# Performance work log

Hardware: AMD Instinct MI355X
Metric: run time of the kernel (lower is better)

The kernel has to match this reference:

```python
import jax, jax.numpy as jnp
import numpy as np

B = 512       # number of graphs
MAX_N = 128   # pad length (>= max(num_atoms))
D = 256       # emb_dim


def setup_inputs() -> dict:
    key = jax.random.key(0)
    ks = jax.random.split(key, 20)
    num_atoms_np = np.full(B, 80, dtype=np.int64)
    num_atoms_np[: B // 2] = 112
    num_atoms_np[B // 2 :] = 48
    total = int(num_atoms_np.sum())  # 40960, static
    scale = 1.0 / np.sqrt(D)

    def lin_w(k):
        return jax.random.normal(k, (D, D), jnp.float32) * scale

    inp = {
        'rep_2d': jax.random.normal(ks[0], (total, D), jnp.float32),
        'rep_3d': jax.random.normal(ks[1], (total, D), jnp.float32),
        'num_atoms': jnp.asarray(num_atoms_np),
        # mha_2d_3d (queries from 2d, keys/values from 3d)
        'wq23': lin_w(ks[2]), 'bq23': jnp.zeros((D,), jnp.float32),
        'wk23': lin_w(ks[3]), 'bk23': jnp.zeros((D,), jnp.float32),
        'wv23': lin_w(ks[4]), 'bv23': jnp.zeros((D,), jnp.float32),
        # mha_3d_2d (queries from 3d, keys/values from 2d)
        'wq32': lin_w(ks[5]), 'bq32': jnp.zeros((D,), jnp.float32),
        'wk32': lin_w(ks[6]), 'bk32': jnp.zeros((D,), jnp.float32),
        'wv32': lin_w(ks[7]), 'bv32': jnp.zeros((D,), jnp.float32),
        # per-branch Linear (normalizer=Identity) + GELU
        'wm23': lin_w(ks[8]), 'bm23': jnp.zeros((D,), jnp.float32),
        'wm32': lin_w(ks[9]), 'bm32': jnp.zeros((D,), jnp.float32),
    }
    return inp


def _variadic_to_padded(flat, num_atoms):
    # flat: [total, D] -> padded [B, MAX_N, D], mask [B, MAX_N] (True = valid)
    cum = jnp.cumsum(num_atoms)
    offsets = cum - num_atoms
    pos = jnp.arange(MAX_N)
    mask = pos[None, :] < num_atoms[:, None]
    idx = jnp.where(mask, offsets[:, None] + pos[None, :], 0)
    padded = flat[idx] * mask[..., None].astype(flat.dtype)
    return padded, mask


def _padded_to_variadic(padded, num_atoms, total):
    # padded: [B, MAX_N, D] -> flat [total, D]
    cum = jnp.cumsum(num_atoms)
    t = jnp.arange(total)
    b = jnp.searchsorted(cum, t, side='right')
    i = t - (cum - num_atoms)[b]
    return padded[b, i]


def _cross_attn(q_in, kv_in, mask, wq, bq, wk, bk, wv, bv):
    # single-head scaled dot-product cross-attention, key-side padding mask
    q = q_in @ wq.T + bq
    k = kv_in @ wk.T + bk
    v = kv_in @ wv.T + bv
    s = jnp.einsum('bqd,bkd->bqk', q, k) / jnp.sqrt(jnp.asarray(D, q.dtype))
    s = jnp.where(mask[:, None, :], s, jnp.asarray(-1e9, s.dtype))
    a = jax.nn.softmax(s, axis=-1)
    return jnp.einsum('bqk,bkd->bqd', a, v)


def reference(rep_2d, rep_3d, num_atoms,
              wq23, bq23, wk23, bk23, wv23, bv23,
              wq32, bq32, wk32, bk32, wv32, bv32,
              wm23, bm23, wm32, bm32):
    total = rep_2d.shape[0]
    p2d, mask = _variadic_to_padded(rep_2d, num_atoms)
    p3d, _ = _variadic_to_padded(rep_3d, num_atoms)
    x2d = _cross_attn(p2d, p3d, mask, wq23, bq23, wk23, bk23, wv23, bv23)
    x3d = _cross_attn(p3d, p2d, mask, wq32, bq32, wk32, bk32, wv32, bv32)
    x2d = _padded_to_variadic(x2d, num_atoms, total)
    x3d = _padded_to_variadic(x3d, num_atoms, total)
    out2d = jax.nn.gelu(x2d @ wm23.T + bm23, approximate=False)
    out3d = jax.nn.gelu(x3d @ wm32.T + bm32, approximate=False)
    return (out2d, out3d)
```

## Files before the change

kernel.cpp:

```cpp
#include <hip/hip_runtime.h>
#include <hip/hip_bf16.h>
#include <cstdint>


typedef short s16x8 __attribute__((ext_vector_type(8)));
typedef float f32x4 __attribute__((ext_vector_type(4)));

__device__ __forceinline__ s16x8 cvt8(const float* p) {
  float4 a0 = *(const float4*)p, a1 = *(const float4*)(p + 4);
  union { s16x8 v; __bf16 e[8]; } u;
  u.e[0] = (__bf16)a0.x; u.e[1] = (__bf16)a0.y; u.e[2] = (__bf16)a0.z; u.e[3] = (__bf16)a0.w;
  u.e[4] = (__bf16)a1.x; u.e[5] = (__bf16)a1.y; u.e[6] = (__bf16)a1.z; u.e[7] = (__bf16)a1.w;
  return u.v;
}
__device__ __forceinline__ float fast_gelu(float x) {
  float ax = fabsf(x);
  float t = 1.0f / (1.0f + 0.3275911f * (ax * 0.70710678f));
  float y = t * (0.254829592f + t * (-0.284496736f + t * (1.421413741f +
            t * (-1.453152027f + t * 1.061405429f))));
  float er = 1.0f - y * __expf(-0.5f * ax * ax);
  er = (x < 0.f) ? -er : er;
  return 0.5f * x * (1.0f + er);
}

__global__ void sentinel_kernel(float* out, float v) {
  if (threadIdx.x == 0 && blockIdx.x == 0) out[0] = v;
}

__global__ __launch_bounds__(512) void scan_kernel(
    const int* __restrict__ na, int* __restrict__ offs,
    int B, int total, float* out)
{
  __shared__ int s32[512];
  __shared__ int s64[512];
  const int t = threadIdx.x;
  int v32 = 0, v64 = 0;
  if (t < B) {
    v32 = na[t];
    v64 = (int)((const long long*)na)[t];
  }
  s32[t] = v32; s64[t] = v64;
  __syncthreads();
  for (int o = 1; o < 512; o <<= 1) {
    int a = (t >= o) ? s32[t - o] : 0;
    int b = (t >= o) ? s64[t - o] : 0;
    __syncthreads();
    s32[t] += a; s64[t] += b;
    __syncthreads();
  }
  int tot32 = s32[B - 1], tot64 = s64[B - 1];
  bool ok32 = (tot32 == total), ok64 = (tot64 == total);
  if (t < B) offs[t] = ok32 ? (s32[t] - v32) : ok64 ? (s64[t] - v64) : 0;
  if (t == 0) {
    offs[B] = ok32 ? tot32 : ok64 ? tot64 : 0;
    if (!ok32 && !ok64) out[0] = 31337.0f;
  }
}

__global__ __launch_bounds__(256) void cvt2_kernel(
    const float* __restrict__ in0, const float* __restrict__ in1,
    __bf16* __restrict__ out0, __bf16* __restrict__ out1) {
  const float* in = blockIdx.y ? in1 : in0;
  __bf16* out = blockIdx.y ? out1 : out0;
  int i = (blockIdx.x * 256 + threadIdx.x) * 4;
  float4 f = *(const float4*)(in + i);
  out[i + 0] = (__bf16)f.x; out[i + 1] = (__bf16)f.y;
  out[i + 2] = (__bf16)f.z; out[i + 3] = (__bf16)f.w;
}

__global__ __launch_bounds__(256) void gemm_kernel(
    const float* __restrict__ A, const float* __restrict__ Bw,
    const float* __restrict__ bias, __bf16* __restrict__ C, int N)
{
  __shared__ __bf16 At[128 * 32];
  __shared__ __bf16 Bt[128 * 32];
  const int t = threadIdx.x;
  const int lane = t & 63, w = t >> 6;
  const int wr = w >> 1, wc = w & 1;
  const int l15 = lane & 15, l4 = lane >> 4;
  const int by = blockIdx.x, bx = blockIdx.y;

  f32x4 acc[4][4];
  for (int m = 0; m < 4; ++m)
    for (int nn = 0; nn < 4; ++nn) acc[m][nn] = (f32x4){0.f, 0.f, 0.f, 0.f};

  for (int kk = 0; kk < 256; kk += 32) {
    for (int j = 0; j < 2; ++j) {
      int c = t + j * 256;
      int row = c >> 2, off0 = (c & 3) * 8;
      *(s16x8*)(&At[row * 32 + off0]) = cvt8(A + (size_t)(by * 128 + row) * 256 + kk + off0);
      *(s16x8*)(&Bt[row * 32 + off0]) = cvt8(Bw + (size_t)(bx * 128 + row) * 256 + kk + off0);
    }
    __syncthreads();
    s16x8 af[4], bfr[4];
    for (int m = 0; m < 4; ++m)
      af[m] = *(const s16x8*)(&At[(wr * 64 + m * 16 + l15) * 32 + l4 * 8]);
    for (int nn = 0; nn < 4; ++nn)
      bfr[nn] = *(const s16x8*)(&Bt[(wc * 64 + nn * 16 + l15) * 32 + l4 * 8]);
    for (int m = 0; m < 4; ++m)
      for (int nn = 0; nn < 4; ++nn)
        acc[m][nn] = __builtin_amdgcn_mfma_f32_16x16x32_bf16(af[m], bfr[nn], acc[m][nn], 0, 0, 0);
    __syncthreads();
  }

  for (int m = 0; m < 4; ++m) {
    int row0 = by * 128 + wr * 64 + m * 16 + l4 * 4;
    for (int nn = 0; nn < 4; ++nn) {
      int col = bx * 128 + wc * 64 + nn * 16 + l15;
      float bc = bias[col];
      for (int r = 0; r < 4; ++r) {
        int row = row0 + r;
        C[(size_t)row * N + col] = (__bf16)(acc[m][nn][r] + bc);
      }
    }
  }
}

#define CTP 136
__global__ __launch_bounds__(256) void vgemm_kernel(
    const float* __restrict__ A, const float* __restrict__ Bw,
    const float* __restrict__ bias, __bf16* __restrict__ Vt, int total)
{
  __shared__ __bf16 At[128 * 32];
  __shared__ __bf16 Bt[128 * 32];
  __shared__ __bf16 Ct[128 * CTP];
  const int t = threadIdx.x;
  const int lane = t & 63, w = t >> 6;
  const int wr = w >> 1, wc = w & 1;
  const int l15 = lane & 15, l4 = lane >> 4;
  const int by = blockIdx.x, bx = blockIdx.y;

  f32x4 acc[4][4];
  for (int m = 0; m < 4; ++m)
    for (int nn = 0; nn < 4; ++nn) acc[m][nn] = (f32x4){0.f, 0.f, 0.f, 0.f};

  for (int kk = 0; kk < 256; kk += 32) {
    for (int j = 0; j < 2; ++j) {
      int c = t + j * 256;
      int row = c >> 2, off0 = (c & 3) * 8;
      *(s16x8*)(&At[row * 32 + off0]) = cvt8(A + (size_t)(by * 128 + row) * 256 + kk + off0);
      *(s16x8*)(&Bt[row * 32 + off0]) = cvt8(Bw + (size_t)(bx * 128 + row) * 256 + kk + off0);
    }
    __syncthreads();
    s16x8 af[4], bfr[4];
    for (int m = 0; m < 4; ++m)
      af[m] = *(const s16x8*)(&At[(wr * 64 + m * 16 + l15) * 32 + l4 * 8]);
    for (int nn = 0; nn < 4; ++nn)
      bfr[nn] = *(const s16x8*)(&Bt[(wc * 64 + nn * 16 + l15) * 32 + l4 * 8]);
    for (int m = 0; m < 4; ++m)
      for (int nn = 0; nn < 4; ++nn)
        acc[m][nn] = __builtin_amdgcn_mfma_f32_16x16x32_bf16(af[m], bfr[nn], acc[m][nn], 0, 0, 0);
    __syncthreads();
  }

  for (int m = 0; m < 4; ++m) {
    int rl0 = wr * 64 + m * 16 + l4 * 4;
    for (int nn = 0; nn < 4; ++nn) {
      int cl = wc * 64 + nn * 16 + l15;
      for (int r = 0; r < 4; ++r) {
        int rl = rl0 + r;
        Ct[rl * CTP + cl] = (__bf16)(acc[m][nn][r] + bias[by * 128 + rl]);
      }
    }
  }
  __syncthreads();

  for (int i = 0; i < 8; ++i) {
    int c = t + i * 256;
    int tile = c >> 5, w5 = c & 31;
    int kb_l = tile >> 3, db_l = tile & 7;
    int d_l = w5 & 15, kh = w5 >> 4;
    *(uint4*)(Vt + (((size_t)(bx * 8 + kb_l) * 16 + (by * 8 + db_l)) << 8) + w5 * 8) =
        *(const uint4*)(&Ct[(db_l * 16 + d_l) * CTP + kb_l * 16 + kh * 8]);
  }
}

struct Attn2Args {
  const __bf16* Q[2]; const __bf16* K[2]; const __bf16* V[2];
  unsigned long long X[2];
};
#define KP 264
#define PP 136
#define XP 272
__global__ __launch_bounds__(512, 2) void attn2_kernel(
    Attn2Args args, const int* __restrict__ offs, int total)
{
  __shared__ __bf16 smem[128 * 136];
  __bf16 (*Klds)[KP] = (__bf16(*)[KP])smem;
  __bf16 (*Plds)[PP] = (__bf16(*)[PP])smem;
  __bf16 (*XT)[XP]   = (__bf16(*)[XP])smem;

  const int br = blockIdx.y;
  const __bf16* Q  = args.Q[br];
  const __bf16* Km = args.K[br];
  const __bf16* Vt = args.V[br];
  __bf16* X = (__bf16*)args.X[br];

  const int g = blockIdx.x;
  const int off = offs[g];
  const int n = offs[g + 1] - off;
  const int t = threadIdx.x, lane = t & 63, w = t >> 6;
  const int l15 = lane & 15, l4 = lane >> 4;
  const bool qact = (w * 16) < n;
  const bool big = (n > 64);

  const int srow = t >> 5, scol = (t & 31) * 16;
  uint4 kst[4];
  #pragma unroll
  for (int j = 0; j < 4; ++j)
    kst[j] = *(const uint4*)((const char*)(Km + (size_t)(off + j * 16 + srow) * 256) + scol);
  s16x8 qf[8];
  if (qact) {
    int qr = w * 16 + l15; if (qr >= n) qr = n - 1;
    const __bf16* qp = Q + (size_t)(off + qr) * 256 + l4 * 8;
    #pragma unroll
    for (int kk = 0; kk < 8; ++kk) qf[kk] = *(const s16x8*)(qp + kk * 32);
  }
  #pragma unroll
  for (int j = 0; j < 4; ++j)
    *(uint4*)((char*)&Klds[j * 16 + srow][0] + scol) = kst[j];
  uint4 kst1[4];
  if (big) {
    #pragma unroll
    for (int j = 0; j < 4; ++j)
      kst1[j] = *(const uint4*)((const char*)(Km + (size_t)(off + 64 + j * 16 + srow) * 256) + scol);
  }
  __syncthreads();

  f32x4 sacc[8];
  #pragma unroll
  for (int i = 0; i < 8; ++i) sacc[i] = (f32x4){0.f, 0.f, 0.f, 0.f};
  if (qact) {
    #pragma unroll
    for (int kt = 0; kt < 4; ++kt) {
      const __bf16* kp = &Klds[kt * 16 + l15][l4 * 8];
      #pragma unroll
      for (int kk = 0; kk < 8; ++kk) {
        s16x8 kf = *(const s16x8*)(kp + kk * 32);
        sacc[kt] = __builtin_amdgcn_mfma_f32_16x16x32_bf16(qf[kk], kf, sacc[kt], 0, 0, 0);
      }
    }
  }
  __syncthreads();
  if (big) {
    #pragma unroll
    for (int j = 0; j < 4; ++j)
      *(uint4*)((char*)&Klds[j * 16 + srow][0] + scol) = kst1[j];
    __syncthreads();
    if (qact) {
      #pragma unroll
      for (int kt = 0; kt < 4; ++kt) {
        const __bf16* kp = &Klds[kt * 16 + l15][l4 * 8];
        #pragma unroll
        for (int kk = 0; kk < 8; ++kk) {
          s16x8 kf = *(const s16x8*)(kp + kk * 32);
          sacc[4 + kt] = __builtin_amdgcn_mfma_f32_16x16x32_bf16(qf[kk], kf, sacc[4 + kt], 0, 0, 0);
        }
      }
    }
    __syncthreads();
  }

  if (qact) {
    #pragma unroll
    for (int r = 0; r < 4; ++r) {
      float sv[8];
      float m = -1e30f;
      #pragma unroll
      for (int kt = 0; kt < 8; ++kt) {
        int key = kt * 16 + l15;
        float v = (key < n) ? sacc[kt][r] * 0.0625f : -1e30f;
        sv[kt] = v; m = fmaxf(m, v);
      }
      for (int o = 1; o < 16; o <<= 1) m = fmaxf(m, __shfl_xor(m, o));
      float p[8], sum = 0.f;
      #pragma unroll
      for (int kt = 0; kt < 8; ++kt) { p[kt] = __expf(sv[kt] - m); sum += p[kt]; }
      for (int o = 1; o < 16; o <<= 1) sum += __shfl_xor(sum, o);
      float inv = 1.f / sum;
      int q = w * 16 + l4 * 4 + r;
      #pragma unroll
      for (int kt = 0; kt < 4; ++kt)
        Plds[q][kt * 16 + l15] = (__bf16)(p[kt] * inv);
      if (big) {
        #pragma unroll
        for (int kt = 4; kt < 8; ++kt)
          Plds[q][kt * 16 + l15] = (__bf16)(p[kt] * inv);
      }
    }
  }
  __syncthreads();

  const int dbase = w * 32;
  const int ktiles = total >> 4;
  f32x4 xacc[2][8];
  #pragma unroll
  for (int dt = 0; dt < 2; ++dt)
    #pragma unroll
    for (int qm = 0; qm < 8; ++qm) xacc[dt][qm] = (f32x4){0.f, 0.f, 0.f, 0.f};

  #pragma unroll
  for (int dt = 0; dt < 2; ++dt) {
    int db = w * 2 + dt;
    s16x8 vf[4];
    #pragma unroll
    for (int ks = 0; ks < 4; ++ks) {
      int kb = (off >> 4) + ks * 2 + (l4 >> 1);
      if (kb >= ktiles) kb = ktiles - 1;
      vf[ks] = *(const s16x8*)(Vt + (((size_t)kb * 16 + db) << 8)
                               + (l15 + ((l4 & 1) << 4)) * 8);
    }
    #pragma unroll
    for (int qm = 0; qm < 8; ++qm) {
      #pragma unroll
      for (int ks = 0; ks < 4; ++ks) {
        if (ks * 32 < n) {
          s16x8 pa = *(const s16x8*)(&Plds[qm * 16 + l15][ks * 32 + l4 * 8]);
          xacc[dt][qm] = __builtin_amdgcn_mfma_f32_16x16x32_bf16(pa, vf[ks], xacc[dt][qm], 0, 0, 0);
        }
      }
    }
  }
  __syncthreads();

  #pragma unroll
  for (int dt = 0; dt < 2; ++dt)
    #pragma unroll
    for (int qm = 0; qm < 4; ++qm)
      #pragma unroll
      for (int r = 0; r < 4; ++r)
        XT[qm * 16 + l4 * 4 + r][dbase + dt * 16 + l15] = (__bf16)xacc[dt][qm][r];
  __syncthreads();
  #pragma unroll
  for (int i = 0; i < 4; ++i) {
    int c = t + i * 512;
    int row = c >> 5, seg = c & 31;
    if (row < n)
      *(uint4*)(X + (size_t)(off + row) * 256 + seg * 8) =
          *(const uint4*)(&XT[row][seg * 8]);
  }
  if (big) {
    __syncthreads();
    #pragma unroll
    for (int dt = 0; dt < 2; ++dt)
      #pragma unroll
      for (int qm = 4; qm < 8; ++qm)
        #pragma unroll
        for (int r = 0; r < 4; ++r)
          XT[(qm - 4) * 16 + l4 * 4 + r][dbase + dt * 16 + l15] = (__bf16)xacc[dt][qm][r];
    __syncthreads();
    #pragma unroll
    for (int i = 0; i < 4; ++i) {
      int c = t + i * 512;
      int row = c >> 5, seg = c & 31;
      int grow = 64 + row;
      if (grow < n)
        *(uint4*)(X + (size_t)(off + grow) * 256 + seg * 8) =
            *(const uint4*)(&XT[row][seg * 8]);
    }
  }
}

#define OP 88
__global__ __launch_bounds__(256) void gemm_out(
    const __bf16* __restrict__ A, const __bf16* __restrict__ W,
    const float* __restrict__ bias, float* __restrict__ C)
{
  __shared__ __bf16 At[64 * OP];
  __shared__ __bf16 Bt[128 * OP];
  const int t = threadIdx.x;
  const int lane = t & 63, w = t >> 6;
  const int wr = w >> 1, wc = w & 1;
  const int l15 = lane & 15, l4 = lane >> 4;
  const int by = blockIdx.x, bx = blockIdx.y;

  f32x4 acc[2][4];
  for (int m = 0; m < 2; ++m)
    for (int nn = 0; nn < 4; ++nn) acc[m][nn] = (f32x4){0.f, 0.f, 0.f, 0.f};

  for (int kk = 0; kk < 256; kk += 64) {
    #pragma unroll
    for (int j = 0; j < 2; ++j) {
      int c = t + j * 256;
      int row = c >> 3, off0 = (c & 7) * 8;
      *(s16x8*)(&At[row * OP + off0]) =
          *(const s16x8*)(A + (size_t)(by * 64 + row) * 256 + kk + off0);
    }
    #pragma unroll
    for (int j = 0; j < 4; ++j) {
      int c = t + j * 256;
      int row = c >> 3, off0 = (c & 7) * 8;
      *(s16x8*)(&Bt[row * OP + off0]) =
          *(const s16x8*)(W + (size_t)(bx * 128 + row) * 256 + kk + off0);
    }
    __syncthreads();
    #pragma unroll
    for (int k2 = 0; k2 < 2; ++k2) {
      s16x8 af[2], bfr[4];
      #pragma unroll
      for (int m = 0; m < 2; ++m)
        af[m] = *(const s16x8*)(&At[(wr * 32 + m * 16 + l15) * OP + k2 * 32 + l4 * 8]);
      #pragma unroll
      for (int nn = 0; nn < 4; ++nn)
        bfr[nn] = *(const s16x8*)(&Bt[(wc * 64 + nn * 16 + l15) * OP + k2 * 32 + l4 * 8]);
      #pragma unroll
      for (int m = 0; m < 2; ++m)
        #pragma unroll
        for (int nn = 0; nn < 4; ++nn)
          acc[m][nn] = __builtin_amdgcn_mfma_f32_16x16x32_bf16(af[m], bfr[nn], acc[m][nn], 0, 0, 0);
    }
    __syncthreads();
  }

  for (int m = 0; m < 2; ++m) {
    int row0 = by * 64 + wr * 32 + m * 16 + l4 * 4;
    for (int nn = 0; nn < 4; ++nn) {
      int col = bx * 128 + wc * 64 + nn * 16 + l15;
      float bc = bias[col];
      for (int r = 0; r < 4; ++r) {
        int row = row0 + r;
        C[(size_t)row * 256 + col] = fast_gelu(acc[m][nn][r] + bc);
      }
    }
  }
}

extern "C" void kernel_launch(void* const* d_in, const int* in_sizes, int n_in,
                              void* d_out, int out_size, void* d_ws, size_t ws_size,
                              hipStream_t stream) {
  const float* rep2d = (const float*)d_in[0];
  const float* rep3d = (const float*)d_in[1];
  const int*   na    = (const int*)d_in[2];
  const float* wq23 = (const float*)d_in[3];  const float* bq23 = (const float*)d_in[4];
  const float* wk23 = (const float*)d_in[5];  const float* bk23 = (const float*)d_in[6];
  const float* wv23 = (const float*)d_in[7];  const float* bv23 = (const float*)d_in[8];
  const float* wq32 = (const float*)d_in[9];  const float* bq32 = (const float*)d_in[10];
  const float* wk32 = (const float*)d_in[11]; const float* bk32 = (const float*)d_in[12];
  const float* wv32 = (const float*)d_in[13]; const float* bv32 = (const float*)d_in[14];
  const float* wm23 = (const float*)d_in[15]; const float* bm23 = (const float*)d_in[16];
  const float* wm32 = (const float*)d_in[17]; const float* bm32 = (const float*)d_in[18];

  const int B = in_sizes[2];
  const int total = in_sizes[0] / 256;
  float* out = (float*)d_out;

  char* ws = (char*)d_ws;
  const size_t SZ = (size_t)total * 256 * sizeof(__bf16);
  const size_t WMB = 65536 * sizeof(__bf16);
  const size_t need6 = 8192 + 2 * WMB + 6 * SZ;
  const size_t need3 = 8192 + 2 * WMB + 3 * SZ;
  int* offs = (int*)ws;

  dim3 blk(256);
  dim3 blkA(512);
  dim3 gP(total / 128, 2);
  dim3 gV(2, total / 128);
  dim3 gO(total / 64, 2);

  if (ws_size >= need6) {
    __bf16* WM0 = (__bf16*)(ws + 8192);
    __bf16* WM1 = (__bf16*)(ws + 8192 + WMB);
    __bf16* BQ1 = (__bf16*)(ws + 8192 + 2 * WMB);
    __bf16* BK1 = (__bf16*)(ws + 8192 + 2 * WMB + SZ);
    __bf16* BV1 = (__bf16*)(ws + 8192 + 2 * WMB + 2 * SZ);
    __bf16* BQ2 = (__bf16*)(ws + 8192 + 2 * WMB + 3 * SZ);
    __bf16* BK2 = (__bf16*)(ws + 8192 + 2 * WMB + 4 * SZ);
    __bf16* BV2 = (__bf16*)(ws + 8192 + 2 * WMB + 5 * SZ);

    scan_kernel<<<1, 512, 0, stream>>>(na, offs, B, total, out);
    cvt2_kernel<<<dim3(64, 2), blk, 0, stream>>>(wm23, wm32, WM0, WM1);
    gemm_kernel<<<gP, blk, 0, stream>>>(rep2d, wq23, bq23, BQ1, 256);
    gemm_kernel<<<gP, blk, 0, stream>>>(rep3d, wk23, bk23, BK1, 256);
    vgemm_kernel<<<gV, blk, 0, stream>>>(wv23, rep3d, bv23, BV1, total);
    gemm_kernel<<<gP, blk, 0, stream>>>(rep3d, wq32, bq32, BQ2, 256);
    gemm_kernel<<<gP, blk, 0, stream>>>(rep2d, wk32, bk32, BK2, 256);
    vgemm_kernel<<<gV, blk, 0, stream>>>(wv32, rep2d, bv32, BV2, total);

    Attn2Args aa;
    aa.Q[0] = BQ1; aa.K[0] = BK1; aa.V[0] = BV1; aa.X[0] = (unsigned long long)BQ1;
    aa.Q[1] = BQ2; aa.K[1] = BK2; aa.V[1] = BV2; aa.X[1] = (unsigned long long)BQ2;
    attn2_kernel<<<dim3(B, 2), blkA, 0, stream>>>(aa, offs, total);

    gemm_out<<<gO, blk, 0, stream>>>(BQ1, WM0, bm23, out);
    gemm_out<<<gO, blk, 0, stream>>>(BQ2, WM1, bm32, out + (size_t)total * 256);
  } else if (ws_size >= need3) {
    __bf16* WM0 = (__bf16*)(ws + 8192);
    __bf16* WM1 = (__bf16*)(ws + 8192 + WMB);
    __bf16* BQ = (__bf16*)(ws + 8192 + 2 * WMB);
    __bf16* BK = (__bf16*)(ws + 8192 + 2 * WMB + SZ);
    __bf16* BV = (__bf16*)(ws + 8192 + 2 * WMB + 2 * SZ);

    scan_kernel<<<1, 512, 0, stream>>>(na, offs, B, total, out);
    cvt2_kernel<<<dim3(64, 2), blk, 0, stream>>>(wm23, wm32, WM0, WM1);
    for (int br = 0; br < 2; ++br) {
      const float* rq = br ? rep3d : rep2d;
      const float* rk = br ? rep2d : rep3d;
      const float* wq = br ? wq32 : wq23;  const float* bq = br ? bq32 : bq23;
      const float* wk = br ? wk32 : wk23;  const float* bk = br ? bk32 : bk23;
      const float* wv = br ? wv32 : wv23;  const float* bv = br ? bv32 : bv23;
      __bf16* wm = br ? WM1 : WM0;         const float* bm = br ? bm32 : bm23;
      float* o = out + (size_t)br * total * 256;

      gemm_kernel<<<gP, blk, 0, stream>>>(rq, wq, bq, BQ, 256);
      gemm_kernel<<<gP, blk, 0, stream>>>(rk, wk, bk, BK, 256);
      vgemm_kernel<<<gV, blk, 0, stream>>>(wv, rk, bv, BV, total);
      Attn2Args aa;
      aa.Q[0] = BQ; aa.K[0] = BK; aa.V[0] = BV; aa.X[0] = (unsigned long long)BQ;
      aa.Q[1] = BQ; aa.K[1] = BK; aa.V[1] = BV; aa.X[1] = (unsigned long long)BQ;
      attn2_kernel<<<dim3(B, 1), blkA, 0, stream>>>(aa, offs, total);
      gemm_out<<<gO, blk, 0, stream>>>(BQ, wm, bm, o);
    }
  } else {
    sentinel_kernel<<<1, 64, 0, stream>>>(out, 54321.0f);
  }
}
```

Baseline: 204.9 us.

## Remap block-to-tile order for attention, V-GEMM and output GEMM locality

The scan kernel now builds a permutation of graphs grouped by (offset>>7)&7, so consecutive attention blocks, which land on different XCDs in round-robin, handle graphs whose data maps to the same L2/XCD partition as the earlier producer blocks. The V-GEMM grid is transposed so row tiles vary fastest, and gemm_out gets an XCD-aware swizzle of row-tile indices. The aim is better cache locality across the MI355X XCDs' separate L2s. The cost is a serial single-thread permutation loop in the scan kernel.

```diff
diff --git a/kernel.cpp b/kernel.cpp
--- a/kernel.cpp
+++ b/kernel.cpp
@@ -28,7 +28,7 @@
 }
 
 __global__ __launch_bounds__(512) void scan_kernel(
-    const int* __restrict__ na, int* __restrict__ offs,
+    const int* __restrict__ na, int* __restrict__ offs, int* __restrict__ perm,
     int B, int total, float* out)
 {
   __shared__ int s32[512];
@@ -54,6 +54,24 @@
   if (t == 0) {
     offs[B] = ok32 ? tot32 : ok64 ? tot64 : 0;
     if (!ok32 && !ok64) out[0] = 31337.0f;
+  }
+  __syncthreads();
+
+  if (t == 0) {
+    int cap[8], used[8];
+    for (int k = 0; k < 8; ++k) {
+      cap[k] = (B > k) ? ((B - 1 - k) / 8 + 1) : 0;
+      used[k] = 0;
+    }
+    int nl = 0;
+    for (int g = 0; g < B; ++g) {
+      int k = (offs[g] >> 7) & 7;
+      if (used[k] < cap[k]) { perm[k + 8 * used[k]] = g; used[k]++; }
+      else s32[nl++] = g;
+    }
+    int li = 0;
+    for (int k = 0; k < 8; ++k)
+      for (int j = used[k]; j < cap[k]; ++j) perm[k + 8 * j] = s32[li++];
   }
 }
 
@@ -128,7 +146,8 @@
   const int lane = t & 63, w = t >> 6;
   const int wr = w >> 1, wc = w & 1;
   const int l15 = lane & 15, l4 = lane >> 4;
-  const int by = blockIdx.x, bx = blockIdx.y;
+  const int by = blockIdx.y;
+  const int bx = blockIdx.x;
 
   f32x4 acc[4][4];
   for (int m = 0; m < 4; ++m)
@@ -183,7 +202,8 @@
 #define PP 136
 #define XP 272
 __global__ __launch_bounds__(512, 2) void attn2_kernel(
-    Attn2Args args, const int* __restrict__ offs, int total)
+    Attn2Args args, const int* __restrict__ offs, const int* __restrict__ perm,
+    int total)
 {
   __shared__ __bf16 smem[128 * 136];
   __bf16 (*Klds)[KP] = (__bf16(*)[KP])smem;
@@ -196,7 +216,7 @@
   const __bf16* Vt = args.V[br];
   __bf16* X = (__bf16*)args.X[br];
 
-  const int g = blockIdx.x;
+  const int g = perm[blockIdx.x];
   const int off = offs[g];
   const int n = offs[g + 1] - off;
   const int t = threadIdx.x, lane = t & 63, w = t >> 6;
@@ -364,7 +384,7 @@
 #define OP 88
 __global__ __launch_bounds__(256) void gemm_out(
     const __bf16* __restrict__ A, const __bf16* __restrict__ W,
-    const float* __restrict__ bias, float* __restrict__ C)
+    const float* __restrict__ bias, float* __restrict__ C, int swz)
 {
   __shared__ __bf16 At[64 * OP];
   __shared__ __bf16 Bt[128 * OP];
@@ -372,7 +392,12 @@
   const int lane = t & 63, w = t >> 6;
   const int wr = w >> 1, wc = w & 1;
   const int l15 = lane & 15, l4 = lane >> 4;
-  const int by = blockIdx.x, bx = blockIdx.y;
+  int b = blockIdx.x, by;
+  if (swz) {
+    int k = b & 7, q = b >> 3;
+    by = ((k + ((q >> 1) << 3)) << 1) | (q & 1);
+  } else by = b;
+  const int bx = blockIdx.y;
 
   f32x4 acc[2][4];
   for (int m = 0; m < 2; ++m)
@@ -450,12 +475,14 @@
   const size_t need6 = 8192 + 2 * WMB + 6 * SZ;
   const size_t need3 = 8192 + 2 * WMB + 3 * SZ;
   int* offs = (int*)ws;
+  int* perm = (int*)(ws + 4096);
 
   dim3 blk(256);
   dim3 blkA(512);
   dim3 gP(total / 128, 2);
-  dim3 gV(2, total / 128);
+  dim3 gV(total / 128, 2);
   dim3 gO(total / 64, 2);
+  const int swz = ((total / 64) % 16 == 0) ? 1 : 0;
 
   if (ws_size >= need6) {
     __bf16* WM0 = (__bf16*)(ws + 8192);
@@ -467,7 +494,7 @@
     __bf16* BK2 = (__bf16*)(ws + 8192 + 2 * WMB + 4 * SZ);
     __bf16* BV2 = (__bf16*)(ws + 8192 + 2 * WMB + 5 * SZ);
 
-    scan_kernel<<<1, 512, 0, stream>>>(na, offs, B, total, out);
+    scan_kernel<<<1, 512, 0, stream>>>(na, offs, perm, B, total, out);
     cvt2_kernel<<<dim3(64, 2), blk, 0, stream>>>(wm23, wm32, WM0, WM1);
     gemm_kernel<<<gP, blk, 0, stream>>>(rep2d, wq23, bq23, BQ1, 256);
     gemm_kernel<<<gP, blk, 0, stream>>>(rep3d, wk23, bk23, BK1, 256);
@@ -479,10 +506,10 @@
     Attn2Args aa;
     aa.Q[0] = BQ1; aa.K[0] = BK1; aa.V[0] = BV1; aa.X[0] = (unsigned long long)BQ1;
     aa.Q[1] = BQ2; aa.K[1] = BK2; aa.V[1] = BV2; aa.X[1] = (unsigned long long)BQ2;
-    attn2_kernel<<<dim3(B, 2), blkA, 0, stream>>>(aa, offs, total);
-
-    gemm_out<<<gO, blk, 0, stream>>>(BQ1, WM0, bm23, out);
-    gemm_out<<<gO, blk, 0, stream>>>(BQ2, WM1, bm32, out + (size_t)total * 256);
+    attn2_kernel<<<dim3(B, 2), blkA, 0, stream>>>(aa, offs, perm, total);
+
+    gemm_out<<<gO, blk, 0, stream>>>(BQ1, WM0, bm23, out, swz);
+    gemm_out<<<gO, blk, 0, stream>>>(BQ2, WM1, bm32, out + (size_t)total * 256, swz);
   } else if (ws_size >= need3) {
     __bf16* WM0 = (__bf16*)(ws + 8192);
     __bf16* WM1 = (__bf16*)(ws + 8192 + WMB);
@@ -490,7 +517,7 @@
     __bf16* BK = (__bf16*)(ws + 8192 + 2 * WMB + SZ);
     __bf16* BV = (__bf16*)(ws + 8192 + 2 * WMB + 2 * SZ);
 
-    scan_kernel<<<1, 512, 0, stream>>>(na, offs, B, total, out);
+    scan_kernel<<<1, 512, 0, stream>>>(na, offs, perm, B, total, out);
     cvt2_kernel<<<dim3(64, 2), blk, 0, stream>>>(wm23, wm32, WM0, WM1);
     for (int br = 0; br < 2; ++br) {
       const float* rq = br ? rep3d : rep2d;
@@ -507,8 +534,8 @@
       Attn2Args aa;
       aa.Q[0] = BQ; aa.K[0] = BK; aa.V[0] = BV; aa.X[0] = (unsigned long long)BQ;
       aa.Q[1] = BQ; aa.K[1] = BK; aa.V[1] = BV; aa.X[1] = (unsigned long long)BQ;
-      attn2_kernel<<<dim3(B, 1), blkA, 0, stream>>>(aa, offs, total);
-      gemm_out<<<gO, blk, 0, stream>>>(BQ, wm, bm, o);
+      attn2_kernel<<<dim3(B, 1), blkA, 0, stream>>>(aa, offs, perm, total);
+      gemm_out<<<gO, blk, 0, stream>>>(BQ, wm, bm, o, swz);
     }
   } else {
     sentinel_kernel<<<1, 64, 0, stream>>>(out, 54321.0f);
```

After: 304.1 us. +48.4%, slower.
